# Kernel optimization log

Hardware: AMD Instinct MI355X
Metric: run time of the kernel (lower is better)

## Reference

```python
import jax, jax.numpy as jnp
import numpy as np


def setup_inputs() -> dict:
    key = jax.random.key(0)
    ks = jax.random.split(key, 10)
    B, HD, CD = 8192, 1024, 1024
    stdv = 1.0 / np.sqrt(HD)
    inp = {
        "hprev": jax.random.normal(ks[0], (B, HD), dtype=jnp.float32),
        "cprev": jax.random.normal(ks[1], (B, CD), dtype=jnp.float32),
        "w_hi": jax.random.uniform(ks[2], (HD, CD), jnp.float32, -stdv, stdv),
        "b_hi": jax.random.uniform(ks[3], (1, CD), jnp.float32, -stdv, stdv),
        "w_hf": jax.random.uniform(ks[4], (HD, CD), jnp.float32, -stdv, stdv),
        "b_hf": jax.random.uniform(ks[5], (1, CD), jnp.float32, -stdv, stdv),
        "w_hg": jax.random.uniform(ks[6], (HD, CD), jnp.float32, -stdv, stdv),
        "b_hg": jax.random.uniform(ks[7], (1, CD), jnp.float32, -stdv, stdv),
        "w_ho": jax.random.uniform(ks[8], (HD, CD), jnp.float32, -stdv, stdv),
        "b_ho": jax.random.uniform(ks[9], (1, CD), jnp.float32, -stdv, stdv),
    }
    return inp


def reference(hprev, cprev, w_hi, b_hi, w_hf, b_hf, w_hg, b_hg, w_ho, b_ho):
    # LSTM cell gates driven only by previous hidden state.
    i = jax.nn.sigmoid(hprev @ w_hi + b_hi)   # input gate  [B, CD]
    f = jax.nn.sigmoid(hprev @ w_hf + b_hf)   # forget gate [B, CD]
    g = jnp.tanh(hprev @ w_hg + b_hg)         # cell candidate
    o = jax.nn.sigmoid(hprev @ w_ho + b_ho)   # output gate
    cprime = f * cprev + i * g
    hprime = o * jnp.tanh(cprime)
    return (hprime, cprime)
```

## Files before the change

### kernel.cpp

```cpp
#include <hip/hip_runtime.h>
#include <hip/hip_bf16.h>
#include <stdint.h>

typedef short short8 __attribute__((ext_vector_type(8)));
typedef float f32x4 __attribute__((ext_vector_type(4)));

#define MDIM 8192
#define KDIM 1024
#define NDIM 1024
#define NKT  16


__device__ __forceinline__ unsigned short f2bf(float f) {
  union { float f; unsigned int u; } v; v.f = f;
  unsigned int u = v.u;
  u += 0x7fffu + ((u >> 16) & 1u);
  return (unsigned short)(u >> 16);
}

__device__ __forceinline__ void load_lds16(const void* gsrc, void* ldst) {
  __builtin_amdgcn_global_load_lds(
      (__attribute__((address_space(1))) void*)gsrc,
      (__attribute__((address_space(3))) void*)ldst,
      16, 0, 0);
}

__device__ __forceinline__ float fast_sigmoid(float x) {
  return 1.0f / (1.0f + __expf(-x));
}

__device__ __forceinline__ float fast_tanh(float x) {
  x = fminf(30.0f, fmaxf(-30.0f, x));
  float e = __expf(-2.0f * x);
  return (1.0f - e) / (1.0f + e);
}


__global__ void convert_h_tiled(const float* __restrict__ in,
                                unsigned short* __restrict__ out, int nchunk) {
  int idx = blockIdx.x * blockDim.x + threadIdx.x;
  int stride = gridDim.x * blockDim.x;
  for (int i = idx; i < nchunk; i += stride) {
    int r = i >> 7;
    int kc8 = i & 127;
    const float4* src = reinterpret_cast<const float4*>(in + (size_t)r * KDIM + kc8 * 8);
    float4 v0 = src[0], v1 = src[1];
    short8 o;
    o[0] = (short)f2bf(v0.x); o[1] = (short)f2bf(v0.y);
    o[2] = (short)f2bf(v0.z); o[3] = (short)f2bf(v0.w);
    o[4] = (short)f2bf(v1.x); o[5] = (short)f2bf(v1.y);
    o[6] = (short)f2bf(v1.z); o[7] = (short)f2bf(v1.w);
    int kt = kc8 >> 3;
    int c8 = kc8 & 7;
    reinterpret_cast<short8*>(out)[((size_t)kt * MDIM + r) * 8 + c8] = o;
  }
}

__global__ void convert_w_tiled(const float* __restrict__ w0,
                                const float* __restrict__ w1,
                                const float* __restrict__ w2,
                                const float* __restrict__ w3,
                                unsigned short* __restrict__ out) {
  __shared__ float tile[64][65];
  int g = blockIdx.z;
  const float* w = (g == 0) ? w0 : (g == 1) ? w1 : (g == 2) ? w2 : w3;
  int kt = blockIdx.y;
  int k0 = kt * 64;
  int n0 = blockIdx.x * 64;
  int tx = threadIdx.x;
  int ty = threadIdx.y;
#pragma unroll
  for (int j = 0; j < 16; ++j) {
    int kk = ty * 16 + j;
    tile[kk][tx] = w[(size_t)(k0 + kk) * NDIM + n0 + tx];
  }
  __syncthreads();
#pragma unroll
  for (int j = 0; j < 16; ++j) {
    int nn = ty * 16 + j;
    out[(((size_t)kt * 4 + g) * NDIM + n0 + nn) * 64 + tx] = f2bf(tile[tx][nn]);
  }
}


#define X0 0
#define X1 65536

#define BAR() __builtin_amdgcn_s_barrier()
#define LGKM0() do { \
    asm volatile("s_waitcnt lgkmcnt(0)" ::: "memory"); \
    __builtin_amdgcn_sched_barrier(0); } while (0)
#define VM6() asm volatile("s_waitcnt vmcnt(6)" ::: "memory")

#define STG_A(BUF, ktv, h) do { \
    const uint32_t _oA = ((uint32_t)(ktv) << 20) + srcA + (h) * 16384; \
    load_lds16(ab + _oA,        ldsb + (BUF) + (h) * 16384 + tid * 16); \
    load_lds16(ab + _oA + 8192, ldsb + (BUF) + (h) * 16384 + 8192 + tid * 16); } while (0)
#define STG_B(BUF, ktv, h) do { \
    const uint32_t _oB = ((uint32_t)(ktv) << 19) + srcB0 + (h) * 262144; \
    load_lds16(bb + _oB,          ldsb + (BUF) + 32768 + (h) * 16384 + tid * 16); \
    load_lds16(bb + _oB + 131072, ldsb + (BUF) + 32768 + (h) * 16384 + 8192 + tid * 16); } while (0)

#define LDB_ALL(CB) do { \
    _Pragma("unroll") for (int g = 0; g < 4; ++g) { \
      Br[g * 2 + 0] = *(const short8*)(ldsb + (CB) + b_base + g * 8192 + s0v); \
      Br[g * 2 + 1] = *(const short8*)(ldsb + (CB) + b_base + g * 8192 + s1v); } } while (0)
#define LDA_Q(CB, qm) do { \
    _Pragma("unroll") for (int f = 0; f < 4; ++f) { \
      Ar[f * 2 + 0] = *(const short8*)(ldsb + (CB) + a_base + ((qm) * 64 + f * 16) * 128 + s0v); \
      Ar[f * 2 + 1] = *(const short8*)(ldsb + (CB) + a_base + ((qm) * 64 + f * 16) * 128 + s1v); } } while (0)

#define MFMAQ(qm, qn) do { \
    __builtin_amdgcn_s_setprio(1); \
    _Pragma("unroll") for (int kk = 0; kk < 2; ++kk) \
    _Pragma("unroll") for (int f = 0; f < 4; ++f) \
    _Pragma("unroll") for (int gg = 0; gg < 2; ++gg) \
      acc[(qn) * 2 + gg][(qm) * 4 + f] = __builtin_amdgcn_mfma_f32_16x16x32_bf16( \
          Ar[f * 2 + kk], Br[((qn) * 2 + gg) * 2 + kk], \
          acc[(qn) * 2 + gg][(qm) * 4 + f], 0, 0, 0); \
    __builtin_amdgcn_s_setprio(0); } while (0)

#define BLOCK4(CB, OB, tA1, tN2) do { \
     \
    LDB_ALL(CB); LDA_Q(CB, 0); \
    STG_A(OB, tA1, 1); \
    BAR(); LGKM0(); MFMAQ(0, 0); BAR(); \
     \
    STG_B(CB, tN2, 0); \
    BAR(); MFMAQ(0, 1); BAR(); \
     \
    LDA_Q(CB, 1); \
    STG_B(CB, tN2, 1); \
    BAR(); LGKM0(); MFMAQ(1, 0); BAR(); \
     \
    STG_A(CB, tN2, 0); \
    BAR(); MFMAQ(1, 1); VM6(); BAR(); } while (0)

__global__ __launch_bounds__(512, 2) void lstm_fused_gemm(
    const unsigned short* __restrict__ At,
    const unsigned short* __restrict__ Bt,
    const float* __restrict__ cprev,
    const float* __restrict__ b_i, const float* __restrict__ b_f,
    const float* __restrict__ b_g, const float* __restrict__ b_o,
    float* __restrict__ out)
{
  extern __shared__ unsigned char ldsb[];
  const int tid  = threadIdx.x;
  const int lane = tid & 63;
  const int wave = tid >> 6;
  const int wr = wave >> 2;
  const int wc = wave & 3;
  const int r15 = lane & 15;
  const int hh  = lane >> 4;

  int bid = blockIdx.x;
  int loc = bid >> 3;
  int nb = (bid & 7) * 2 + (loc >> 5);
  int mb = loc & 31;
  int brow = mb * 256;
  int bcol = nb * 64;

  const char* ab = (const char*)At;
  const char* bb = (const char*)Bt;

  const int srow = tid >> 3;
  const int cx = (((tid & 7) ^ (srow & 7)) << 4);
  const uint32_t srcA  = (uint32_t)(brow + srow) * 128 + cx;
  const uint32_t srcB0 = (uint32_t)(bcol + srow) * 128 + cx;

  const uint32_t a_base = (uint32_t)(wr * 128 + r15) * 128;
  const uint32_t b_base = 32768u + (uint32_t)(wc * 16 + r15) * 128;
  const int s0v = ((hh ^ (r15 & 7)) << 4);
  const int s1v = s0v ^ 64;

  f32x4 acc[4][8];
#pragma unroll
  for (int g = 0; g < 4; ++g)
#pragma unroll
    for (int m = 0; m < 8; ++m)
      acc[g][m] = (f32x4){0.f, 0.f, 0.f, 0.f};

  short8 Ar[8], Br[8];

  STG_A(X0, 0, 0); STG_A(X0, 0, 1);
  STG_B(X0, 0, 0); STG_B(X0, 0, 1);
  STG_B(X1, 1, 0); STG_B(X1, 1, 1);
  STG_A(X1, 1, 0);
  VM6();
  BAR();

  for (int it = 0; it < NKT / 2; ++it) {
    const int t0 = 2 * it;
    BLOCK4(X0, X1, (t0 + 1) & 15, (t0 + 2) & 15);
    BLOCK4(X1, X0, (t0 + 2) & 15, (t0 + 3) & 15);
  }

  const size_t outC = (size_t)MDIM * NDIM;
  const int cc = bcol + wc * 16 + r15;
  const float bi = b_i[cc], bff = b_f[cc], bg = b_g[cc], bo = b_o[cc];
#pragma unroll
  for (int m = 0; m < 8; ++m) {
#pragma unroll
    for (int j = 0; j < 4; ++j) {
      int rr = brow + wr * 128 + m * 16 + hh * 4 + j;
      size_t base = (size_t)rr * NDIM + cc;
      float pi = acc[0][m][j] + bi;
      float pf = acc[1][m][j] + bff;
      float pg = acc[2][m][j] + bg;
      float po = acc[3][m][j] + bo;
      float iv = fast_sigmoid(pi);
      float fv = fast_sigmoid(pf);
      float gv = fast_tanh(pg);
      float ov = fast_sigmoid(po);
      float cp = fv * cprev[base] + iv * gv;
      float hp = ov * fast_tanh(cp);
      out[base] = hp;
      out[outC + base] = cp;
    }
  }
}


extern "C" void kernel_launch(void* const* d_in, const int* in_sizes, int n_in,
                              void* d_out, int out_size, void* d_ws, size_t ws_size,
                              hipStream_t stream) {
  const float* hprev = (const float*)d_in[0];
  const float* cprev = (const float*)d_in[1];
  const float* w_hi  = (const float*)d_in[2];
  const float* b_hi  = (const float*)d_in[3];
  const float* w_hf  = (const float*)d_in[4];
  const float* b_hf  = (const float*)d_in[5];
  const float* w_hg  = (const float*)d_in[6];
  const float* b_hg  = (const float*)d_in[7];
  const float* w_ho  = (const float*)d_in[8];
  const float* b_ho  = (const float*)d_in[9];
  float* out = (float*)d_out;

  unsigned short* At = (unsigned short*)d_ws;
  unsigned short* Bt = (unsigned short*)((char*)d_ws + (size_t)NKT * MDIM * 64 * 2);

  convert_h_tiled<<<2048, 256, 0, stream>>>(hprev, At, MDIM * KDIM / 8);
  convert_w_tiled<<<dim3(16, 16, 4), dim3(64, 4, 1), 0, stream>>>(
      w_hi, w_hf, w_hg, w_ho, Bt);
  lstm_fused_gemm<<<512, 512, 131072, stream>>>(At, Bt, cprev,
                                                b_hi, b_hf, b_hg, b_ho, out);
}
```

Measured before the change: 105.6 us.

## Make GEMM blocks persistent over two row tiles with continuous prefetch

Halves the grid to 256 workgroups. Each one now computes two consecutive 256-row tiles, running a single 32-step virtual K loop. Prefetch of the second tile's A/B slices overlaps the first tile's tail and epilogue, which hides pipeline fill/drain costs. The trade-off is that the epilogue now stalls the MFMA pipeline mid-loop, and with 256 blocks on 256 CUs there is one block per CU instead of two, so occupancy drops.

```diff
diff --git a/kernel.cpp b/kernel.cpp
--- a/kernel.cpp
+++ b/kernel.cpp
@@ -92,12 +92,14 @@
     __builtin_amdgcn_sched_barrier(0); } while (0)
 #define VM6() asm volatile("s_waitcnt vmcnt(6)" ::: "memory")
 
-#define STG_A(BUF, ktv, h) do { \
-    const uint32_t _oA = ((uint32_t)(ktv) << 20) + srcA + (h) * 16384; \
+#define STG_A(BUF, vt, h) do { \
+    const uint32_t _vv = (uint32_t)(vt) & 31u; \
+    const uint32_t _oA = ((_vv & 15u) << 20) + ((_vv >> 4) << 15) + srcA + (h) * 16384; \
     load_lds16(ab + _oA,        ldsb + (BUF) + (h) * 16384 + tid * 16); \
     load_lds16(ab + _oA + 8192, ldsb + (BUF) + (h) * 16384 + 8192 + tid * 16); } while (0)
-#define STG_B(BUF, ktv, h) do { \
-    const uint32_t _oB = ((uint32_t)(ktv) << 19) + srcB0 + (h) * 262144; \
+#define STG_B(BUF, vt, h) do { \
+    const uint32_t _vv = (uint32_t)(vt) & 15u; \
+    const uint32_t _oB = (_vv << 19) + srcB0 + (h) * 262144; \
     load_lds16(bb + _oB,          ldsb + (BUF) + 32768 + (h) * 16384 + tid * 16); \
     load_lds16(bb + _oB + 131072, ldsb + (BUF) + 32768 + (h) * 16384 + 8192 + tid * 16); } while (0)
 
@@ -121,20 +123,37 @@
     __builtin_amdgcn_s_setprio(0); } while (0)
 
 #define BLOCK4(CB, OB, tA1, tN2) do { \
-     \
     LDB_ALL(CB); LDA_Q(CB, 0); \
     STG_A(OB, tA1, 1); \
     BAR(); LGKM0(); MFMAQ(0, 0); BAR(); \
-     \
     STG_B(CB, tN2, 0); \
     BAR(); MFMAQ(0, 1); BAR(); \
-     \
     LDA_Q(CB, 1); \
     STG_B(CB, tN2, 1); \
     BAR(); LGKM0(); MFMAQ(1, 0); BAR(); \
-     \
     STG_A(CB, tN2, 0); \
     BAR(); MFMAQ(1, 1); VM6(); BAR(); } while (0)
+
+#define EPILOG(brow_) do { \
+    const int cc = bcol + wc * 16 + r15; \
+    const float bi = b_i[cc], bff = b_f[cc], bg = b_g[cc], bo = b_o[cc]; \
+    _Pragma("unroll") for (int m = 0; m < 8; ++m) { \
+      _Pragma("unroll") for (int j = 0; j < 4; ++j) { \
+        int rr = (brow_) + wr * 128 + m * 16 + hh * 4 + j; \
+        size_t base = (size_t)rr * NDIM + cc; \
+        float pi = acc[0][m][j] + bi; \
+        float pf = acc[1][m][j] + bff; \
+        float pg = acc[2][m][j] + bg; \
+        float po = acc[3][m][j] + bo; \
+        float iv = fast_sigmoid(pi); \
+        float fv = fast_sigmoid(pf); \
+        float gv = fast_tanh(pg); \
+        float ov = fast_sigmoid(po); \
+        float cp = fv * cprev[base] + iv * gv; \
+        float hp = ov * fast_tanh(cp); \
+        out[base] = hp; \
+        out[outC + base] = cp; \
+      } } } while (0)
 
 __global__ __launch_bounds__(512, 2) void lstm_fused_gemm(
     const unsigned short* __restrict__ At,
@@ -155,9 +174,10 @@
 
   int bid = blockIdx.x;
   int loc = bid >> 3;
-  int nb = (bid & 7) * 2 + (loc >> 5);
-  int mb = loc & 31;
-  int brow = mb * 256;
+  int nb = (bid & 7) * 2 + (loc >> 4);
+  int mbp = loc & 15;
+  int brow0 = mbp * 512;
+  int brow1 = brow0 + 256;
   int bcol = nb * 64;
 
   const char* ab = (const char*)At;
@@ -165,13 +185,15 @@
 
   const int srow = tid >> 3;
   const int cx = (((tid & 7) ^ (srow & 7)) << 4);
-  const uint32_t srcA  = (uint32_t)(brow + srow) * 128 + cx;
+  const uint32_t srcA  = (uint32_t)(brow0 + srow) * 128 + cx;
   const uint32_t srcB0 = (uint32_t)(bcol + srow) * 128 + cx;
 
   const uint32_t a_base = (uint32_t)(wr * 128 + r15) * 128;
   const uint32_t b_base = 32768u + (uint32_t)(wc * 16 + r15) * 128;
   const int s0v = ((hh ^ (r15 & 7)) << 4);
   const int s1v = s0v ^ 64;
+
+  const size_t outC = (size_t)MDIM * NDIM;
 
   f32x4 acc[4][8];
 #pragma unroll
@@ -189,35 +211,21 @@
   VM6();
   BAR();
 
-  for (int it = 0; it < NKT / 2; ++it) {
-    const int t0 = 2 * it;
-    BLOCK4(X0, X1, (t0 + 1) & 15, (t0 + 2) & 15);
-    BLOCK4(X1, X0, (t0 + 2) & 15, (t0 + 3) & 15);
-  }
-
-  const size_t outC = (size_t)MDIM * NDIM;
-  const int cc = bcol + wc * 16 + r15;
-  const float bi = b_i[cc], bff = b_f[cc], bg = b_g[cc], bo = b_o[cc];
-#pragma unroll
-  for (int m = 0; m < 8; ++m) {
-#pragma unroll
-    for (int j = 0; j < 4; ++j) {
-      int rr = brow + wr * 128 + m * 16 + hh * 4 + j;
-      size_t base = (size_t)rr * NDIM + cc;
-      float pi = acc[0][m][j] + bi;
-      float pf = acc[1][m][j] + bff;
-      float pg = acc[2][m][j] + bg;
-      float po = acc[3][m][j] + bo;
-      float iv = fast_sigmoid(pi);
-      float fv = fast_sigmoid(pf);
-      float gv = fast_tanh(pg);
-      float ov = fast_sigmoid(po);
-      float cp = fv * cprev[base] + iv * gv;
-      float hp = ov * fast_tanh(cp);
-      out[base] = hp;
-      out[outC + base] = cp;
+  for (int vp = 0; vp < 16; ++vp) {
+    const int v = 2 * vp;
+    BLOCK4(X0, X1, v + 1, v + 2);
+    BLOCK4(X1, X0, v + 2, v + 3);
+    if (vp == 7) {
+      EPILOG(brow0);
+#pragma unroll
+      for (int g = 0; g < 4; ++g)
+#pragma unroll
+        for (int m = 0; m < 8; ++m)
+          acc[g][m] = (f32x4){0.f, 0.f, 0.f, 0.f};
     }
   }
+
+  EPILOG(brow1);
 }
 
 
@@ -242,6 +250,6 @@
   convert_h_tiled<<<2048, 256, 0, stream>>>(hprev, At, MDIM * KDIM / 8);
   convert_w_tiled<<<dim3(16, 16, 4), dim3(64, 4, 1), 0, stream>>>(
       w_hi, w_hf, w_hg, w_ho, Bt);
-  lstm_fused_gemm<<<512, 512, 131072, stream>>>(At, Bt, cprev,
+  lstm_fused_gemm<<<256, 512, 131072, stream>>>(At, Bt, cprev,
                                                 b_hi, b_hf, b_hg, b_ho, out);
 }
```

Result: slower. 153.0 us (+44.9%).
